# Kernel optimization log

Measured on AMD Instinct MI355X. Metric: run time of the kernel, lower is better.

Reference implementation:

```python
import jax, jax.numpy as jnp
import numpy as np

N = 50_000       # nodes
E = 1_600_000    # edges per edge set (avg degree 32)
D = 128          # hidden dim
F_IN = 1273      # fixed num_features in NetGIN
G = 512          # graphs in batch
STEPS = 6        # Set2Set processing steps
BN_EPS = 1e-5


def setup_inputs() -> dict:
    key = jax.random.key(0)
    ks = iter(jax.random.split(key, 40))
    def rn(shape, fan_in):
        return jax.random.normal(next(ks), shape, jnp.float32) / np.float32(np.sqrt(fan_in))
    inp = {}
    inp["x"] = jax.random.normal(next(ks), (N, F_IN), jnp.float32)
    for i in (1, 2, 3):
        inp[f"edge_index_{i}"] = jax.random.randint(next(ks), (2, E), 0, N, jnp.int32)
    inp["batch"] = jnp.sort(jax.random.randint(next(ks), (N,), 0, G, jnp.int32))
    # GINConv MLPs: layer 1 has input F_IN, layers 2-6 have input D
    inp["conv1_W1"] = rn((3, F_IN, D), F_IN)
    inp["conv1_b1"] = jnp.zeros((3, D), jnp.float32)
    inp["conv_rest_W1"] = rn((5, 3, D, D), D)
    inp["conv_rest_b1"] = jnp.zeros((5, 3, D), jnp.float32)
    inp["conv_W2"] = rn((6, 3, D, D), D)
    inp["conv_b2"] = jnp.zeros((6, 3, D), jnp.float32)
    inp["conv_bn1_g"] = jnp.ones((6, 3, D), jnp.float32)
    inp["conv_bn1_b"] = jnp.zeros((6, 3, D), jnp.float32)
    inp["conv_bn2_g"] = jnp.ones((6, 3, D), jnp.float32)
    inp["conv_bn2_b"] = jnp.zeros((6, 3, D), jnp.float32)
    inp["conv_eps"] = jnp.zeros((6, 3), jnp.float32)  # train_eps=True, init 0
    # fusion MLPs (3*D -> D -> D)
    inp["mlp_W1"] = rn((6, 3 * D, D), 3 * D)
    inp["mlp_b1"] = jnp.zeros((6, D), jnp.float32)
    inp["mlp_bn1_g"] = jnp.ones((6, D), jnp.float32)
    inp["mlp_bn1_b"] = jnp.zeros((6, D), jnp.float32)
    inp["mlp_W2"] = rn((6, D, D), D)
    inp["mlp_b2"] = jnp.zeros((6, D), jnp.float32)
    inp["mlp_bn2_g"] = jnp.ones((6, D), jnp.float32)
    inp["mlp_bn2_b"] = jnp.zeros((6, D), jnp.float32)
    # Set2Set single-layer LSTM: input 2D, hidden D; gate order i,f,g,o
    inp["lstm_Wih"] = rn((4 * D, 2 * D), 2 * D)
    inp["lstm_Whh"] = rn((4 * D, D), D)
    inp["lstm_bih"] = jnp.zeros((4 * D,), jnp.float32)
    inp["lstm_bhh"] = jnp.zeros((4 * D,), jnp.float32)
    inp["fc1_W"] = rn((2 * D, D), 2 * D)
    inp["fc1_b"] = jnp.zeros((D,), jnp.float32)
    inp["fc4_W"] = rn((D, 12), D)
    inp["fc4_b"] = jnp.zeros((12,), jnp.float32)
    return inp


def _bn(x, g, b):
    # BatchNorm1d in training mode: batch statistics (biased var), eps=1e-5
    mu = jnp.mean(x, axis=0)
    var = jnp.var(x, axis=0)
    return g * (x - mu) * jax.lax.rsqrt(var + BN_EPS) + b


def _mlp2(h, W1, b1, g1, bb1, W2, b2, g2, bb2):
    h = jax.nn.relu(_bn(h @ W1 + b1, g1, bb1))
    return jax.nn.relu(_bn(h @ W2 + b2, g2, bb2))


def _gin(h, ei, eps, W1, b1, g1, bb1, W2, b2, g2, bb2):
    # sum-aggregate neighbor features: out[dst] += h[src]
    agg = jax.ops.segment_sum(h[ei[0]], ei[1], num_segments=h.shape[0])
    return _mlp2((1.0 + eps) * h + agg, W1, b1, g1, bb1, W2, b2, g2, bb2)


def _forward(x, conv1_W1, conv1_b1, conv_rest_W1, conv_rest_b1, conv_W2, conv_b2,
             conv_bn1_g, conv_bn1_b, conv_bn2_g, conv_bn2_b, conv_eps,
             mlp_W1, mlp_b1, mlp_bn1_g, mlp_bn1_b, mlp_W2, mlp_b2, mlp_bn2_g, mlp_bn2_b,
             lstm_Wih, lstm_Whh, lstm_bih, lstm_bhh, fc1_W, fc1_b, fc4_W, fc4_b,
             edge_index_1, edge_index_2, edge_index_3, batch):
    edges = (edge_index_1, edge_index_2, edge_index_3)
    h = x
    for l in range(6):
        xs = []
        for k in range(3):
            W1 = conv1_W1[k] if l == 0 else conv_rest_W1[l - 1, k]
            b1 = conv1_b1[k] if l == 0 else conv_rest_b1[l - 1, k]
            xk = jax.nn.relu(_gin(h, edges[k], conv_eps[l, k], W1, b1,
                                  conv_bn1_g[l, k], conv_bn1_b[l, k],
                                  conv_W2[l, k], conv_b2[l, k],
                                  conv_bn2_g[l, k], conv_bn2_b[l, k]))
            xs.append(xk)
        h = _mlp2(jnp.concatenate(xs, axis=-1),
                  mlp_W1[l], mlp_b1[l], mlp_bn1_g[l], mlp_bn1_b[l],
                  mlp_W2[l], mlp_b2[l], mlp_bn2_g[l], mlp_bn2_b[l])
    # Set2Set readout (processing_steps=6)
    q_star = jnp.zeros((G, 2 * D), h.dtype)
    hh = jnp.zeros((G, D), h.dtype)
    cc = jnp.zeros((G, D), h.dtype)
    for _ in range(STEPS):
        gates = q_star @ lstm_Wih.T + hh @ lstm_Whh.T + lstm_bih + lstm_bhh
        i_g, f_g, g_g, o_g = jnp.split(gates, 4, axis=-1)
        cc = jax.nn.sigmoid(f_g) * cc + jax.nn.sigmoid(i_g) * jnp.tanh(g_g)
        hh = jax.nn.sigmoid(o_g) * jnp.tanh(cc)
        q = hh
        e = jnp.sum(h * q[batch], axis=-1)              # [N]
        emax = jax.ops.segment_max(e, batch, num_segments=G)
        ex = jnp.exp(e - emax[batch])
        denom = jax.ops.segment_sum(ex, batch, num_segments=G)
        a = ex / denom[batch]                            # per-graph softmax
        r = jax.ops.segment_sum(a[:, None] * h, batch, num_segments=G)
        q_star = jnp.concatenate([q, r], axis=-1)
    out = jax.nn.relu(q_star @ fc1_W + fc1_b)
    return out @ fc4_W + fc4_b                           # [G, 12]


def reference(x, conv1_W1, conv1_b1, conv_rest_W1, conv_rest_b1, conv_W2, conv_b2,
              conv_bn1_g, conv_bn1_b, conv_bn2_g, conv_bn2_b, conv_eps,
              mlp_W1, mlp_b1, mlp_bn1_g, mlp_bn1_b, mlp_W2, mlp_b2, mlp_bn2_g, mlp_bn2_b,
              lstm_Wih, lstm_Whh, lstm_bih, lstm_bhh, fc1_W, fc1_b, fc4_W, fc4_b,
              edge_index_1, edge_index_2, edge_index_3, batch):
    return _forward(x, conv1_W1, conv1_b1, conv_rest_W1, conv_rest_b1, conv_W2, conv_b2,
                    conv_bn1_g, conv_bn1_b, conv_bn2_g, conv_bn2_b, conv_eps,
                    mlp_W1, mlp_b1, mlp_bn1_g, mlp_bn1_b, mlp_W2, mlp_b2, mlp_bn2_g, mlp_bn2_b,
                    lstm_Wih, lstm_Whh, lstm_bih, lstm_bhh, fc1_W, fc1_b, fc4_W, fc4_b,
                    edge_index_1, edge_index_2, edge_index_3, batch)
```

## Files before the change

kernel.cpp:

```cpp
#include <hip/hip_runtime.h>
#include <cstdint>
#include <cstddef>

#define NN 50000
#define EE 1600000
#define GG 512
#define FIN 1273

typedef unsigned short u16;
typedef unsigned int u32;
typedef __attribute__((ext_vector_type(8))) short short8;
typedef __attribute__((ext_vector_type(4))) float f32x4;

__device__ __forceinline__ float sigmf(float x) { return 1.f / (1.f + expf(-x)); }

__device__ __forceinline__ void splitbf(float v, u16& hi, u16& lo) {
    const u32 u = __float_as_uint(v);
    hi = (u16)(u >> 16);
    const float rem = v - __uint_as_float(u & 0xffff0000u);
    lo = (u16)(__float_as_uint(rem) >> 16);
}

__device__ __forceinline__ void gload_lds16(const void* g, void* l) {
    __builtin_amdgcn_global_load_lds(
        (const __attribute__((address_space(1))) void*)g,
        (__attribute__((address_space(3))) void*)l, 16, 0, 0);
}

__device__ __forceinline__ bool remap3(int f, int nRow, int& mat, int& rt) {
    const int g = f / 24, w = f - g * 24;
    rt = g * 8 + (w & 7);
    mat = w >> 3;
    return rt < nRow;
}

__global__ __launch_bounds__(256) void gemm_l0(
    const float* __restrict__ A, int lda, int K, int Kreal,
    const u16* __restrict__ Bhi, const u16* __restrict__ Blo, size_t strideB,
    float* __restrict__ C, int ldc, int coffStep, int M, int nRow)
{
    __shared__ u16 lsAhi[128 * 64];
    __shared__ u16 lsAlo[128 * 64];
    __shared__ u16 lsBhi[128 * 64];
    __shared__ u16 lsBlo[128 * 64];
    int mat, rt;
    if (!remap3(blockIdx.x, nRow, mat, rt)) return;
    const int tid = threadIdx.x;
    const int wave = tid >> 6, lane = tid & 63;
    const int row0 = rt * 128;
    const int coff = mat * coffStep;
    const u16* Bh = Bhi + (size_t)mat * strideB;
    const u16* Bl = Blo + (size_t)mat * strideB;
    const int wm = wave >> 1, wn = wave & 1;
    f32x4 acc[4][4] = {};

    for (int k0 = 0; k0 < K; k0 += 64) {
        if (k0) __syncthreads();
        #pragma unroll
        for (int i = 0; i < 4; ++i) {
            const int slot = i * 256 + tid;
            const int r = slot >> 3, ch = tid & 7;
            int gr = row0 + r; if (gr >= M) gr = M - 1;
            const int kb = k0 + ch * 8;
            u16 th[8], tl[8];
            const float* src = A + (size_t)gr * lda + kb;
            if (kb + 8 <= Kreal) {
                const float4 v0 = *(const float4*)(src);
                const float4 v1 = *(const float4*)(src + 4);
                const float va[8] = {v0.x, v0.y, v0.z, v0.w,
                                     v1.x, v1.y, v1.z, v1.w};
                #pragma unroll
                for (int e = 0; e < 8; ++e) splitbf(va[e], th[e], tl[e]);
            } else {
                #pragma unroll
                for (int e = 0; e < 8; ++e) {
                    const float v = (kb + e < Kreal) ? src[e] : 0.f;
                    splitbf(v, th[e], tl[e]);
                }
            }
            const int off = (r << 6) + ((ch ^ (r & 7)) << 3);
            *(short8*)&lsAhi[off] = *(const short8*)th;
            *(short8*)&lsAlo[off] = *(const short8*)tl;
        }
        #pragma unroll
        for (int i = 0; i < 4; ++i) {
            const int slot = i * 256 + wave * 64 + lane;
            const int r = slot >> 3, ch = slot & 7;
            const int sch = ch ^ (r & 7);
            const size_t goff = (size_t)r * K + k0 + sch * 8;
            const int lbase = (i * 256 + wave * 64) * 8;
            gload_lds16(Bh + goff, &lsBhi[lbase]);
            gload_lds16(Bl + goff, &lsBlo[lbase]);
        }
        __syncthreads();
        #pragma unroll
        for (int ks = 0; ks < 2; ++ks) {
            short8 ah[4], al[4], bh[4], bl[4];
            const int kch = ks * 4 + (lane >> 4);
            #pragma unroll
            for (int m = 0; m < 4; ++m) {
                const int r = wm * 64 + m * 16 + (lane & 15);
                const int off = (r << 6) + ((kch ^ (r & 7)) << 3);
                ah[m] = *(const short8*)&lsAhi[off];
                al[m] = *(const short8*)&lsAlo[off];
            }
            #pragma unroll
            for (int n = 0; n < 4; ++n) {
                const int c = wn * 64 + n * 16 + (lane & 15);
                const int off = (c << 6) + ((kch ^ (c & 7)) << 3);
                bh[n] = *(const short8*)&lsBhi[off];
                bl[n] = *(const short8*)&lsBlo[off];
            }
            #pragma unroll
            for (int m = 0; m < 4; ++m)
                #pragma unroll
                for (int n = 0; n < 4; ++n) {
                    acc[m][n] = __builtin_amdgcn_mfma_f32_16x16x32_bf16(
                        ah[m], bh[n], acc[m][n], 0, 0, 0);
                    acc[m][n] = __builtin_amdgcn_mfma_f32_16x16x32_bf16(
                        ah[m], bl[n], acc[m][n], 0, 0, 0);
                    acc[m][n] = __builtin_amdgcn_mfma_f32_16x16x32_bf16(
                        al[m], bh[n], acc[m][n], 0, 0, 0);
                }
        }
    }
    #pragma unroll
    for (int n = 0; n < 4; ++n) {
        const int c = wn * 64 + n * 16 + (lane & 15);
        #pragma unroll
        for (int m = 0; m < 4; ++m) {
            #pragma unroll
            for (int j = 0; j < 4; ++j) {
                const int gr = row0 + wm * 64 + m * 16 + ((lane >> 4) << 2) + j;
                if (gr < M)
                    C[(size_t)gr * ldc + coff + c] = acc[m][n][j];
            }
        }
    }
}

__global__ __launch_bounds__(256) void gemm_dir(
    const float* __restrict__ A, size_t strideA, int lda, int K,
    const float* __restrict__ st, int stSlice, int stMat,
    const float* __restrict__ ga, const float* __restrict__ be,
    int gbSlice, int gbMat,
    const u16* __restrict__ Bhi, const u16* __restrict__ Blo, size_t strideB,
    const float* __restrict__ bias, int biasMat,
    float* __restrict__ C, int ldc, int coffStep,
    int M, int do_stats, float* __restrict__ stats_out, int ostatMat,
    int nMat, int nRow)
{
    __shared__ u16 lsBhi[128 * 64];
    __shared__ u16 lsBlo[128 * 64];
    int mat, rt;
    if (nMat == 3) {
        if (!remap3(blockIdx.x, nRow, mat, rt)) return;
    } else { mat = 0; rt = blockIdx.x; }
    const int tid = threadIdx.x;
    const int wave = tid >> 6, lane = tid & 63;
    const int row0 = rt * 128;
    const int wm = wave >> 1, wn = wave & 1;
    A += (size_t)mat * strideA;
    st += mat * stMat; ga += mat * gbMat; be += mat * gbMat;
    if (bias) bias += mat * biasMat;
    if (do_stats) stats_out += mat * ostatMat;
    const u16* Bh = Bhi + (size_t)mat * strideB;
    const u16* Bl = Blo + (size_t)mat * strideB;
    const int coff = mat * coffStep;
    f32x4 acc[4][4] = {};

    int arow[4];
    #pragma unroll
    for (int m = 0; m < 4; ++m) {
        int r = row0 + wm * 64 + m * 16 + (lane & 15);
        if (r >= M) r = M - 1;
        arow[m] = r;
    }

    for (int k0 = 0; k0 < K; k0 += 64) {
        if (k0) __syncthreads();
        #pragma unroll
        for (int i = 0; i < 4; ++i) {
            const int slot = i * 256 + wave * 64 + lane;
            const int r = slot >> 3, ch = slot & 7;
            const int sch = ch ^ (r & 7);
            const size_t goff = (size_t)r * K + k0 + sch * 8;
            const int lbase = (i * 256 + wave * 64) * 8;
            gload_lds16(Bh + goff, &lsBhi[lbase]);
            gload_lds16(Bl + goff, &lsBlo[lbase]);
        }
        __syncthreads();
        #pragma unroll
        for (int ks = 0; ks < 2; ++ks) {
            const int kch = ks * 4 + (lane >> 4);
            const int kb = k0 + kch * 8;
            float scv[8], shv[8];
            {
                const int s = kb >> 7, d0 = kb & 127;
                const float* stS = st + s * stSlice;
                const float* gS  = ga + s * gbSlice;
                const float* beS = be + s * gbSlice;
                #pragma unroll
                for (int e = 0; e < 8; ++e) {
                    const int d = d0 + e;
                    const float mu = stS[d] * (1.f / NN);
                    const float var = fmaxf(stS[128 + d] * (1.f / NN) - mu * mu, 0.f);
                    const float sc = gS[d] * rsqrtf(var + 1e-5f);
                    scv[e] = sc;
                    shv[e] = beS[d] - sc * mu;
                }
            }
            short8 ah[4], al[4];
            #pragma unroll
            for (int m = 0; m < 4; ++m) {
                const float* src = A + (size_t)arow[m] * lda + kb;
                const float4 v0 = *(const float4*)(src);
                const float4 v1 = *(const float4*)(src + 4);
                const float va[8] = {v0.x, v0.y, v0.z, v0.w,
                                     v1.x, v1.y, v1.z, v1.w};
                u16 th[8], tl[8];
                #pragma unroll
                for (int e = 0; e < 8; ++e) {
                    const float y = fmaxf(fmaf(scv[e], va[e], shv[e]), 0.f);
                    splitbf(y, th[e], tl[e]);
                }
                ah[m] = *(const short8*)th;
                al[m] = *(const short8*)tl;
            }
            #pragma unroll
            for (int n = 0; n < 4; ++n) {
                const int c = wn * 64 + n * 16 + (lane & 15);
                const int off = (c << 6) + ((kch ^ (c & 7)) << 3);
                const short8 bh = *(const short8*)&lsBhi[off];
                const short8 bl = *(const short8*)&lsBlo[off];
                #pragma unroll
                for (int m = 0; m < 4; ++m) {
                    acc[m][n] = __builtin_amdgcn_mfma_f32_16x16x32_bf16(
                        ah[m], bh, acc[m][n], 0, 0, 0);
                    acc[m][n] = __builtin_amdgcn_mfma_f32_16x16x32_bf16(
                        ah[m], bl, acc[m][n], 0, 0, 0);
                    acc[m][n] = __builtin_amdgcn_mfma_f32_16x16x32_bf16(
                        al[m], bh, acc[m][n], 0, 0, 0);
                }
            }
        }
    }

    float colsum[4] = {0.f, 0.f, 0.f, 0.f}, colsq[4] = {0.f, 0.f, 0.f, 0.f};
    #pragma unroll
    for (int n = 0; n < 4; ++n) {
        const int c = wn * 64 + n * 16 + (lane & 15);
        const float bv = bias ? bias[c] : 0.f;
        #pragma unroll
        for (int m = 0; m < 4; ++m) {
            #pragma unroll
            for (int j = 0; j < 4; ++j) {
                const int gr = row0 + wm * 64 + m * 16 + ((lane >> 4) << 2) + j;
                if (gr < M) {
                    const float v = acc[m][n][j] + bv;
                    C[(size_t)gr * ldc + coff + c] = v;
                    colsum[n] += v; colsq[n] += v * v;
                }
            }
        }
    }
    if (do_stats) {
        float* ssum = (float*)lsBhi;
        float* ssq  = ssum + 128;
        __syncthreads();
        if (tid < 128) { ssum[tid] = 0.f; ssq[tid] = 0.f; }
        __syncthreads();
        #pragma unroll
        for (int n = 0; n < 4; ++n) {
            const int c = wn * 64 + n * 16 + (lane & 15);
            atomicAdd(&ssum[c], colsum[n]);
            atomicAdd(&ssq[c], colsq[n]);
        }
        __syncthreads();
        if (tid < 128) {
            atomicAdd(&stats_out[tid],       ssum[tid]);
            atomicAdd(&stats_out[128 + tid], ssq[tid]);
        }
    }
}

__global__ __launch_bounds__(256) void wt_cast2(const float* __restrict__ W,
                                                u16* __restrict__ Whi,
                                                u16* __restrict__ Wlo,
                                                int total, int K, int Kpad) {
    const int idx = blockIdx.x * 256 + threadIdx.x;
    if (idx >= total) return;
    const int perm = 128 * Kpad;
    const int m = idx / perm, rem = idx - m * perm;
    const int n = rem / Kpad, k = rem - n * Kpad;
    const float v = (k < K) ? W[(size_t)m * K * 128 + (size_t)k * 128 + n] : 0.f;
    u16 hi, lo;
    splitbf(v, hi, lo);
    Whi[idx] = hi; Wlo[idx] = lo;
}

template <bool BT>
__global__ __launch_bounds__(256) void gemm_f32(
    const float* __restrict__ A, const float* __restrict__ B,
    const float* __restrict__ bias, float* __restrict__ C,
    int M, int K, int Nc)
{
    __shared__ float As[32][68];
    __shared__ float Bs[32][132];
    const int tid = threadIdx.x;
    const int tx = tid & 15, ty = tid >> 4;
    const int row0 = blockIdx.x * 64, col0 = blockIdx.y * 128;
    float acc[4][8] = {};
    for (int k0 = 0; k0 < K; k0 += 32) {
        {
            const int kk = tid & 31, rb = tid >> 5;
            #pragma unroll
            for (int i = 0; i < 8; ++i) {
                const int r = rb + i * 8, gr = row0 + r, gk = k0 + kk;
                As[kk][r] = (gr < M && gk < K) ? A[(size_t)gr * K + gk] : 0.f;
            }
        }
        if (!BT) {
            const int c = tid & 127, kb = tid >> 7;
            #pragma unroll
            for (int i = 0; i < 16; ++i) {
                const int kk = kb + i * 2, gk = k0 + kk;
                Bs[kk][c] = (gk < K) ? B[(size_t)gk * Nc + col0 + c] : 0.f;
            }
        } else {
            const int kk = tid & 31, cb = tid >> 5;
            #pragma unroll
            for (int i = 0; i < 16; ++i) {
                const int c = cb + i * 8, gk = k0 + kk;
                Bs[kk][c] = (gk < K) ? B[(size_t)(col0 + c) * K + gk] : 0.f;
            }
        }
        __syncthreads();
        #pragma unroll 8
        for (int kk = 0; kk < 32; ++kk) {
            const float4 av  = *(const float4*)&As[kk][ty * 4];
            const float4 bv0 = *(const float4*)&Bs[kk][tx * 8];
            const float4 bv1 = *(const float4*)&Bs[kk][tx * 8 + 4];
            const float a[4] = {av.x, av.y, av.z, av.w};
            const float b[8] = {bv0.x, bv0.y, bv0.z, bv0.w, bv1.x, bv1.y, bv1.z, bv1.w};
            #pragma unroll
            for (int i = 0; i < 4; ++i)
                #pragma unroll
                for (int j = 0; j < 8; ++j)
                    acc[i][j] = fmaf(a[i], b[j], acc[i][j]);
        }
        __syncthreads();
    }
    #pragma unroll
    for (int j = 0; j < 8; ++j) {
        const float bv = bias ? bias[col0 + tx * 8 + j] : 0.f;
        #pragma unroll
        for (int i = 0; i < 4; ++i) acc[i][j] += bv;
    }
    #pragma unroll
    for (int i = 0; i < 4; ++i) {
        const int gr = row0 + ty * 4 + i;
        if (gr < M) {
            *(float4*)&C[(size_t)gr * Nc + col0 + tx * 8] =
                make_float4(acc[i][0], acc[i][1], acc[i][2], acc[i][3]);
            *(float4*)&C[(size_t)gr * Nc + col0 + tx * 8 + 4] =
                make_float4(acc[i][4], acc[i][5], acc[i][6], acc[i][7]);
        }
    }
}

__global__ __launch_bounds__(256) void count_deg(const int* __restrict__ dst,
                                                 int* __restrict__ deg) {
    const int e = blockIdx.x * 256 + threadIdx.x;
    if (e < EE) atomicAdd(&deg[dst[e]], 1);
}

__global__ __launch_bounds__(512) void scan1(const int* __restrict__ deg,
                                             int* __restrict__ scanned,
                                             int* __restrict__ bsum) {
    __shared__ int s[512];
    const int t = threadIdx.x;
    const int i = blockIdx.x * 512 + t;
    const int v = (i < NN) ? deg[i] : 0;
    s[t] = v; __syncthreads();
    for (int o = 1; o < 512; o <<= 1) {
        const int tv = (t >= o) ? s[t - o] : 0;
        __syncthreads();
        s[t] += tv;
        __syncthreads();
    }
    if (i < NN) scanned[i] = s[t];
    if (t == 511) bsum[blockIdx.x] = s[511];
}

__global__ __launch_bounds__(128) void scan2(int* __restrict__ bsum, int nb) {
    __shared__ int s[128];
    const int t = threadIdx.x;
    const int v = (t < nb) ? bsum[t] : 0;
    s[t] = v; __syncthreads();
    for (int o = 1; o < 128; o <<= 1) {
        const int tv = (t >= o) ? s[t - o] : 0;
        __syncthreads();
        s[t] += tv;
        __syncthreads();
    }
    if (t < nb) bsum[t] = s[t] - v;
}

__global__ __launch_bounds__(256) void scan3(const int* __restrict__ deg,
                                             const int* __restrict__ scanned,
                                             const int* __restrict__ bsum,
                                             int* __restrict__ rowptr,
                                             int* __restrict__ cursor) {
    const int i = blockIdx.x * 256 + threadIdx.x;
    if (i < NN) {
        const int v = bsum[i >> 9] + scanned[i] - deg[i];
        rowptr[i] = v; cursor[i] = v;
    }
    if (i == 0) rowptr[NN] = EE;
}

__global__ __launch_bounds__(256) void fill_csr(const int* __restrict__ src,
                                                const int* __restrict__ dst,
                                                int* __restrict__ cursor,
                                                int* __restrict__ csrc) {
    const int e = blockIdx.x * 256 + threadIdx.x;
    if (e < EE) {
        const int pos = atomicAdd(&cursor[dst[e]], 1);
        csrc[pos] = src[e];
    }
}

__global__ __launch_bounds__(256) void agg_combine(
    const float* __restrict__ X, int ldp4,
    const int* __restrict__ rowptrB, const int* __restrict__ csrcB,
    const float* __restrict__ b1B,
    const float* __restrict__ eps_arr, int epsBase,
    float* __restrict__ zB, float* __restrict__ statsB)
{
    __shared__ float red[256];
    const int k = blockIdx.y;
    const int* rowptr = rowptrB + (size_t)k * (NN + 1);
    const int* csrc   = csrcB + (size_t)k * EE;
    const float* b1   = b1B + k * 128;
    float* z          = zB + (size_t)k * NN * 128;
    float* stats      = statsB + (size_t)k * 512;
    const int tid = threadIdx.x, lane = tid & 63, wave = tid >> 6;
    const float e1 = 1.f + eps_arr[epsBase + k];
    const int half = lane >> 5;
    const int l32 = lane & 31;
    const float4* p4 = (const float4*)X + k * 32;
    float s[4] = {0.f, 0.f, 0.f, 0.f}, q[4] = {0.f, 0.f, 0.f, 0.f};
    float4 bv = make_float4(0.f, 0.f, 0.f, 0.f);
    if (lane < 32) bv = ((const float4*)b1)[l32];
    red[tid] = 0.f;
    __syncthreads();
    const int nbase = blockIdx.x * 16 + wave * 4;
    for (int t = 0; t < 4; ++t) {
        const int wid = nbase + t;
        const int s0 = rowptr[wid], s1 = rowptr[wid + 1];
        float ax = 0.f, ay = 0.f, az = 0.f, aw = 0.f;
        int j = s0;
        for (; j + 15 < s1; j += 16) {
            const int r0 = csrc[j + half],      r1 = csrc[j + 2 + half];
            const int r2 = csrc[j + 4 + half],  r3 = csrc[j + 6 + half];
            const int r4 = csrc[j + 8 + half],  r5 = csrc[j + 10 + half];
            const int r6 = csrc[j + 12 + half], r7 = csrc[j + 14 + half];
            const float4 v0 = p4[(size_t)r0 * ldp4 + l32];
            const float4 v1 = p4[(size_t)r1 * ldp4 + l32];
            const float4 v2 = p4[(size_t)r2 * ldp4 + l32];
            const float4 v3 = p4[(size_t)r3 * ldp4 + l32];
            const float4 v4 = p4[(size_t)r4 * ldp4 + l32];
            const float4 v5 = p4[(size_t)r5 * ldp4 + l32];
            const float4 v6 = p4[(size_t)r6 * ldp4 + l32];
            const float4 v7 = p4[(size_t)r7 * ldp4 + l32];
            ax += (v0.x + v1.x) + (v2.x + v3.x) + (v4.x + v5.x) + (v6.x + v7.x);
            ay += (v0.y + v1.y) + (v2.y + v3.y) + (v4.y + v5.y) + (v6.y + v7.y);
            az += (v0.z + v1.z) + (v2.z + v3.z) + (v4.z + v5.z) + (v6.z + v7.z);
            aw += (v0.w + v1.w) + (v2.w + v3.w) + (v4.w + v5.w) + (v6.w + v7.w);
        }
        for (; j + 7 < s1; j += 8) {
            const int r0 = csrc[j + half],     r1 = csrc[j + 2 + half];
            const int r2 = csrc[j + 4 + half], r3 = csrc[j + 6 + half];
            const float4 v0 = p4[(size_t)r0 * ldp4 + l32];
            const float4 v1 = p4[(size_t)r1 * ldp4 + l32];
            const float4 v2 = p4[(size_t)r2 * ldp4 + l32];
            const float4 v3 = p4[(size_t)r3 * ldp4 + l32];
            ax += (v0.x + v1.x) + (v2.x + v3.x);
            ay += (v0.y + v1.y) + (v2.y + v3.y);
            az += (v0.z + v1.z) + (v2.z + v3.z);
            aw += (v0.w + v1.w) + (v2.w + v3.w);
        }
        for (; j + 3 < s1; j += 4) {
            const int ra = csrc[j + half];
            const int rb = csrc[j + 2 + half];
            const float4 v0 = p4[(size_t)ra * ldp4 + l32];
            const float4 v1 = p4[(size_t)rb * ldp4 + l32];
            ax += v0.x + v1.x; ay += v0.y + v1.y;
            az += v0.z + v1.z; aw += v0.w + v1.w;
        }
        for (; j + 1 < s1; j += 2) {
            const int ra = csrc[j + half];
            const float4 v0 = p4[(size_t)ra * ldp4 + l32];
            ax += v0.x; ay += v0.y; az += v0.z; aw += v0.w;
        }
        if (j < s1 && half == 0) {
            const float4 v0 = p4[(size_t)csrc[j] * ldp4 + l32];
            ax += v0.x; ay += v0.y; az += v0.z; aw += v0.w;
        }
        ax += __shfl_down(ax, 32, 64);
        ay += __shfl_down(ay, 32, 64);
        az += __shfl_down(az, 32, 64);
        aw += __shfl_down(aw, 32, 64);
        if (lane < 32) {
            const float4 self = p4[(size_t)wid * ldp4 + l32];
            float4 zv;
            zv.x = fmaf(e1, self.x, ax + bv.x);
            zv.y = fmaf(e1, self.y, ay + bv.y);
            zv.z = fmaf(e1, self.z, az + bv.z);
            zv.w = fmaf(e1, self.w, aw + bv.w);
            ((float4*)z)[(size_t)wid * 32 + l32] = zv;
            s[0] += zv.x; s[1] += zv.y; s[2] += zv.z; s[3] += zv.w;
            q[0] += zv.x * zv.x; q[1] += zv.y * zv.y;
            q[2] += zv.z * zv.z; q[3] += zv.w * zv.w;
        }
    }
    if (lane < 32) {
        const int d = l32 * 4;
        #pragma unroll
        for (int c = 0; c < 4; ++c) {
            atomicAdd(&red[d + c], s[c]);
            atomicAdd(&red[128 + d + c], q[c]);
        }
    }
    __syncthreads();
    atomicAdd(&stats[tid], red[tid]);
}

__global__ __launch_bounds__(256) void bn_relu_f32(
    const float* __restrict__ xin, const float* __restrict__ stats,
    const float* __restrict__ gamma, const float* __restrict__ beta,
    float* __restrict__ out)
{
    const size_t i = (size_t)blockIdx.x * 256 + threadIdx.x;
    if (i >= (size_t)NN * 64) return;
    const int d = (int)(i & 63) * 2;
    const float inv_n = 1.f / NN;
    const float mu0 = stats[d] * inv_n,     mu1 = stats[d + 1] * inv_n;
    const float v0 = fmaxf(stats[128 + d] * inv_n - mu0 * mu0, 0.f);
    const float v1 = fmaxf(stats[129 + d] * inv_n - mu1 * mu1, 0.f);
    const float s0 = gamma[d] * rsqrtf(v0 + 1e-5f);
    const float s1 = gamma[d + 1] * rsqrtf(v1 + 1e-5f);
    const float2 xv = ((const float2*)xin)[i];
    const float y0 = fmaxf(fmaf(s0, xv.x - mu0, beta[d]), 0.f);
    const float y1 = fmaxf(fmaf(s1, xv.y - mu1, beta[d + 1]), 0.f);
    ((float2*)out)[i] = make_float2(y0, y1);
}

__global__ __launch_bounds__(256) void seg_starts(const int* __restrict__ batch,
                                                  int* __restrict__ gstart) {
    const int i = blockIdx.x * 256 + threadIdx.x;
    if (i >= NN) return;
    const int b = batch[i];
    if (i == 0) { for (int g = 0; g <= b; ++g) gstart[g] = 0; }
    else {
        const int pb = batch[i - 1];
        for (int g = pb + 1; g <= b; ++g) gstart[g] = i;
    }
    if (i == NN - 1) { for (int g = b + 1; g <= GG; ++g) gstart[g] = NN; }
}

__global__ __launch_bounds__(256) void pack_wcat(const float* __restrict__ Wih,
                                                 const float* __restrict__ Whh,
                                                 float* __restrict__ Wcat) {
    const int i = blockIdx.x * 256 + threadIdx.x;
    if (i >= 512 * 384) return;
    const int j = i / 384, k = i - j * 384;
    Wcat[i] = (k < 256) ? Wih[j * 256 + k] : Whh[j * 128 + (k - 256)];
}

__global__ __launch_bounds__(256) void lstm_kernel(
    const float* __restrict__ gates, const float* __restrict__ bih,
    const float* __restrict__ bhh, float* __restrict__ cc, float* __restrict__ S)
{
    const int i = blockIdx.x * 256 + threadIdx.x;
    if (i >= GG * 128) return;
    const int g = i >> 7, d = i & 127;
    const float* gr = gates + (size_t)g * 512;
    const float ig = gr[d]       + bih[d]       + bhh[d];
    const float fg = gr[128 + d] + bih[128 + d] + bhh[128 + d];
    const float gv = gr[256 + d] + bih[256 + d] + bhh[256 + d];
    const float og = gr[384 + d] + bih[384 + d] + bhh[384 + d];
    const float c  = sigmf(fg) * cc[i] + sigmf(ig) * tanhf(gv);
    const float hv = sigmf(og) * tanhf(c);
    cc[i] = c;
    S[(size_t)g * 384 + d] = hv;
    S[(size_t)g * 384 + 256 + d] = hv;
}

__global__ __launch_bounds__(256) void attend_kernel(
    const float* __restrict__ h, float* __restrict__ S,
    float* __restrict__ ews, const int* __restrict__ gstart)
{
    const int g = blockIdx.x;
    const int rs = gstart[g], re = gstart[g + 1];
    const int tid = threadIdx.x, lane = tid & 63, w = tid >> 6;
    __shared__ float q[128];
    __shared__ float red[8];
    if (tid < 128) q[tid] = S[(size_t)g * 384 + 256 + tid];
    __syncthreads();
    const float2* h2 = (const float2*)h;
    float lmax = -1e30f;
    for (int n = rs + w; n < re; n += 4) {
        const float2 hv = h2[(size_t)n * 64 + lane];
        float p = hv.x * q[2 * lane] + hv.y * q[2 * lane + 1];
        #pragma unroll
        for (int o = 32; o; o >>= 1) p += __shfl_down(p, o, 64);
        if (lane == 0) { ews[n] = p; lmax = fmaxf(lmax, p); }
    }
    if (lane == 0) red[w] = lmax;
    __syncthreads();
    const float m = fmaxf(fmaxf(red[0], red[1]), fmaxf(red[2], red[3]));
    __syncthreads();
    float lsum = 0.f;
    for (int n = rs + tid; n < re; n += 256) {
        const float ex = expf(ews[n] - m);
        ews[n] = ex; lsum += ex;
    }
    #pragma unroll
    for (int o = 32; o; o >>= 1) lsum += __shfl_down(lsum, o, 64);
    if (lane == 0) red[w] = lsum;
    __syncthreads();
    const float denom = red[0] + red[1] + red[2] + red[3];
    if (tid < 128) {
        float acc = 0.f;
        for (int n = rs; n < re; ++n)
            acc = fmaf(ews[n], h[(size_t)n * 128 + tid], acc);
        S[(size_t)g * 384 + 128 + tid] = (denom > 0.f) ? acc / denom : 0.f;
    }
}

__global__ __launch_bounds__(128) void fc1_kernel(const float* __restrict__ S,
                                                  const float* __restrict__ W,
                                                  const float* __restrict__ b,
                                                  float* __restrict__ out1) {
    const int g = blockIdx.x, d = threadIdx.x;
    __shared__ float qs[256];
    qs[d] = S[(size_t)g * 384 + d];
    qs[128 + d] = S[(size_t)g * 384 + 128 + d];
    __syncthreads();
    float acc = b[d];
    for (int k = 0; k < 256; ++k) acc = fmaf(qs[k], W[k * 128 + d], acc);
    out1[(size_t)g * 128 + d] = fmaxf(acc, 0.f);
}

__global__ __launch_bounds__(256) void fc4_kernel(const float* __restrict__ out1,
                                                  const float* __restrict__ W,
                                                  const float* __restrict__ b,
                                                  float* __restrict__ out) {
    const int i = blockIdx.x * 256 + threadIdx.x;
    if (i >= GG * 12) return;
    const int g = i / 12, j = i - g * 12;
    float acc = b[j];
    for (int d = 0; d < 128; ++d)
        acc = fmaf(out1[(size_t)g * 128 + d], W[d * 12 + j], acc);
    out[i] = acc;
}

extern "C" void kernel_launch(void* const* d_in, const int* in_sizes, int n_in,
                              void* d_out, int out_size, void* d_ws, size_t ws_size,
                              hipStream_t stream)
{
    const float* x        = (const float*)d_in[0];
    const int*   eidx[3]  = {(const int*)d_in[1], (const int*)d_in[2], (const int*)d_in[3]};
    const int*   batch    = (const int*)d_in[4];
    const float* conv1_W1     = (const float*)d_in[5];
    const float* conv1_b1     = (const float*)d_in[6];
    const float* conv_rest_W1 = (const float*)d_in[7];
    const float* conv_rest_b1 = (const float*)d_in[8];
    const float* conv_W2      = (const float*)d_in[9];
    const float* conv_b2      = (const float*)d_in[10];
    const float* conv_bn1_g   = (const float*)d_in[11];
    const float* conv_bn1_b   = (const float*)d_in[12];
    const float* conv_bn2_g   = (const float*)d_in[13];
    const float* conv_bn2_b   = (const float*)d_in[14];
    const float* conv_eps     = (const float*)d_in[15];
    const float* mlp_W1       = (const float*)d_in[16];
    const float* mlp_b1       = (const float*)d_in[17];
    const float* mlp_bn1_g    = (const float*)d_in[18];
    const float* mlp_bn1_b    = (const float*)d_in[19];
    const float* mlp_W2       = (const float*)d_in[20];
    const float* mlp_b2       = (const float*)d_in[21];
    const float* mlp_bn2_g    = (const float*)d_in[22];
    const float* mlp_bn2_b    = (const float*)d_in[23];
    const float* lstm_Wih     = (const float*)d_in[24];
    const float* lstm_Whh     = (const float*)d_in[25];
    const float* lstm_bih     = (const float*)d_in[26];
    const float* lstm_bhh     = (const float*)d_in[27];
    const float* fc1_W        = (const float*)d_in[28];
    const float* fc1_b        = (const float*)d_in[29];
    const float* fc4_W        = (const float*)d_in[30];
    const float* fc4_b        = (const float*)d_in[31];
    float* outp = (float*)d_out;

    float* f = (float*)d_ws;
    size_t fo = 0;
    float* X     = f + fo; fo += (size_t)NN * 384;
    float* zs    = f + fo; fo += (size_t)NN * 384;
    float* zm2   = f + fo; fo += (size_t)NN * 128;
    float* ews   = f + fo; fo += NN;
    float* stats = f + fo; fo += 48 * 256;
    float* S     = f + fo; fo += (size_t)GG * 384;
    float* ccb   = f + fo; fo += (size_t)GG * 128;
    float* gates = f + fo; fo += (size_t)GG * 512;
    float* Wcat  = f + fo; fo += (size_t)512 * 384;
    float* hbuf = X;
    fo = (fo + 7) & ~(size_t)7;
    u16* b = (u16*)(f + fo);
    size_t bo = 0;
    u16* c1_hi   = b + bo; bo += (size_t)3 * 128 * 1280;
    u16* c1_lo   = b + bo; bo += (size_t)3 * 128 * 1280;
    u16* rw1_hi  = b + bo; bo += (size_t)15 * 128 * 128;
    u16* rw1_lo  = b + bo; bo += (size_t)15 * 128 * 128;
    u16* w2_hi   = b + bo; bo += (size_t)18 * 128 * 128;
    u16* w2_lo   = b + bo; bo += (size_t)18 * 128 * 128;
    u16* mw1_hi  = b + bo; bo += (size_t)6 * 128 * 384;
    u16* mw1_lo  = b + bo; bo += (size_t)6 * 128 * 384;
    u16* mw2_hi  = b + bo; bo += (size_t)6 * 128 * 128;
    u16* mw2_lo  = b + bo; bo += (size_t)6 * 128 * 128;
    int* ip = (int*)(b + bo);
    size_t io = 0;
    int* rowptr0 = ip + io; io += (size_t)3 * (NN + 1);
    int* csrc0   = ip + io; io += (size_t)3 * EE;
    int* deg     = ip + io; io += NN;
    int* cursor  = ip + io; io += NN;
    int* scanned = ip + io; io += NN;
    int* bsum    = ip + io; io += 128;
    int* gstart  = ip + io; io += GG + 1;
    const size_t need = fo * 4 + bo * 2 + io * 4;
    if (ws_size < need) return;

    const int NBLK_SCAN = (NN + 511) / 512;

    {
        int t;
        t = 3 * 128 * 1280;
        wt_cast2<<<(t + 255) / 256, 256, 0, stream>>>(conv1_W1, c1_hi, c1_lo, t, FIN, 1280);
        t = 15 * 128 * 128;
        wt_cast2<<<(t + 255) / 256, 256, 0, stream>>>(conv_rest_W1, rw1_hi, rw1_lo, t, 128, 128);
        t = 18 * 128 * 128;
        wt_cast2<<<(t + 255) / 256, 256, 0, stream>>>(conv_W2, w2_hi, w2_lo, t, 128, 128);
        t = 6 * 128 * 384;
        wt_cast2<<<(t + 255) / 256, 256, 0, stream>>>(mlp_W1, mw1_hi, mw1_lo, t, 384, 384);
        t = 6 * 128 * 128;
        wt_cast2<<<(t + 255) / 256, 256, 0, stream>>>(mlp_W2, mw2_hi, mw2_lo, t, 128, 128);
    }

    for (int s = 0; s < 3; ++s) {
        int* rowptr = rowptr0 + (size_t)s * (NN + 1);
        int* csrc   = csrc0 + (size_t)s * EE;
        hipMemsetAsync(deg, 0, NN * sizeof(int), stream);
        count_deg<<<(EE + 255) / 256, 256, 0, stream>>>(eidx[s] + EE, deg);
        scan1<<<NBLK_SCAN, 512, 0, stream>>>(deg, scanned, bsum);
        scan2<<<1, 128, 0, stream>>>(bsum, NBLK_SCAN);
        scan3<<<(NN + 255) / 256, 256, 0, stream>>>(deg, scanned, bsum, rowptr, cursor);
        fill_csr<<<(EE + 255) / 256, 256, 0, stream>>>(eidx[s], eidx[s] + EE, cursor, csrc);
    }
    seg_starts<<<(NN + 255) / 256, 256, 0, stream>>>(batch, gstart);
    hipMemsetAsync(stats, 0, 48 * 256 * sizeof(float), stream);
    hipMemsetAsync(S, 0, (size_t)GG * 384 * sizeof(float), stream);
    hipMemsetAsync(ccb, 0, (size_t)GG * 128 * sizeof(float), stream);

    const int G128 = (NN + 127) / 128;
    const int G3   = 24 * ((G128 + 7) / 8);
    const int AGG_GRID = NN / 16;

    for (int l = 0; l < 6; ++l) {
        float* stL    = stats + (size_t)l * 8 * 256;
        float* slotF1 = stL + 6 * 256;
        float* slotF2 = stL + 7 * 256;

        if (l == 0)
            gemm_l0<<<G3, 256, 0, stream>>>(
                x, FIN, 1280, FIN, c1_hi, c1_lo, (size_t)128 * 1280,
                X, 384, 128, NN, G128);
        else
            gemm_dir<<<G3, 256, 0, stream>>>(
                zm2, 0, 128, 128,
                stats + (size_t)((l - 1) * 8 + 7) * 256, 0, 0,
                mlp_bn2_g + (l - 1) * 128, mlp_bn2_b + (l - 1) * 128, 0, 0,
                rw1_hi + (size_t)(l - 1) * 3 * 128 * 128,
                rw1_lo + (size_t)(l - 1) * 3 * 128 * 128, (size_t)128 * 128,
                nullptr, 0, X, 384, 128, NN, 0, nullptr, 0, 3, G128);

        {
            const float* b1B = (l == 0) ? conv1_b1 : conv_rest_b1 + (l - 1) * 3 * 128;
            agg_combine<<<dim3(AGG_GRID, 3), 256, 0, stream>>>(
                X, 96, rowptr0, csrc0, b1B, conv_eps, l * 3, zs, stL);
        }

        gemm_dir<<<G3, 256, 0, stream>>>(
            zs, (size_t)NN * 128, 128, 128,
            stL, 0, 512,
            conv_bn1_g + l * 3 * 128, conv_bn1_b + l * 3 * 128, 0, 128,
            w2_hi + (size_t)l * 3 * 128 * 128,
            w2_lo + (size_t)l * 3 * 128 * 128, (size_t)128 * 128,
            conv_b2 + l * 3 * 128, 128,
            X, 384, 128, NN, 1, stL + 256, 512, 3, G128);

        gemm_dir<<<G128, 256, 0, stream>>>(
            X, 0, 384, 384,
            stL + 256, 512, 0,
            conv_bn2_g + l * 3 * 128, conv_bn2_b + l * 3 * 128, 128, 0,
            mw1_hi + (size_t)l * 128 * 384, mw1_lo + (size_t)l * 128 * 384, 0,
            mlp_b1 + l * 128, 0, zs, 128, 0, NN, 1, slotF1, 0, 1, G128);

        gemm_dir<<<G128, 256, 0, stream>>>(
            zs, 0, 128, 128,
            slotF1, 0, 0,
            mlp_bn1_g + l * 128, mlp_bn1_b + l * 128, 0, 0,
            mw2_hi + (size_t)l * 128 * 128, mw2_lo + (size_t)l * 128 * 128, 0,
            mlp_b2 + l * 128, 0, zm2, 128, 0, NN, 1, slotF2, 0, 1, G128);
    }
    bn_relu_f32<<<(NN * 64 + 255) / 256, 256, 0, stream>>>(
        zm2, stats + (size_t)(5 * 8 + 7) * 256,
        mlp_bn2_g + 5 * 128, mlp_bn2_b + 5 * 128, hbuf);

    pack_wcat<<<(512 * 384 + 255) / 256, 256, 0, stream>>>(lstm_Wih, lstm_Whh, Wcat);
    for (int t = 0; t < 6; ++t) {
        gemm_f32<true><<<dim3(8, 4), 256, 0, stream>>>(
            S, Wcat, nullptr, gates, GG, 384, 512);
        lstm_kernel<<<(GG * 128 + 255) / 256, 256, 0, stream>>>(
            gates, lstm_bih, lstm_bhh, ccb, S);
        attend_kernel<<<GG, 256, 0, stream>>>(hbuf, S, ews, gstart);
    }
    fc1_kernel<<<GG, 128, 0, stream>>>(S, fc1_W, fc1_b, gates);
    fc4_kernel<<<(GG * 12 + 255) / 256, 256, 0, stream>>>(gates, fc4_W, fc4_b, outp);
}
```

Before: 5.202 ms.

## Aggregate before first conv linear for layers 1-5 to shrink gather width

For layers after the first, the neighbor aggregation now gathers 128-wide rows from the previous MLP output, applying its BN+ReLU on the fly, instead of gathering the three 384-wide projected rows. The first conv linear (W1) then runs after aggregation as a per-edge-set GEMM, using linearity, and its stats come from that GEMM's epilogue. This cuts the scattered gather volume per layer and removes the pre-aggregation GEMM, but adds a GEMM step and rearranges buffer use. The first layer keeps the original order.

```diff
diff --git a/kernel.cpp b/kernel.cpp
--- a/kernel.cpp
+++ b/kernel.cpp
@@ -139,6 +139,7 @@
     }
 }
 
+template <int ABN>
 __global__ __launch_bounds__(256) void gemm_dir(
     const float* __restrict__ A, size_t strideA, int lda, int K,
     const float* __restrict__ st, int stSlice, int stMat,
@@ -161,7 +162,7 @@
     const int row0 = rt * 128;
     const int wm = wave >> 1, wn = wave & 1;
     A += (size_t)mat * strideA;
-    st += mat * stMat; ga += mat * gbMat; be += mat * gbMat;
+    if (ABN) { st += mat * stMat; ga += mat * gbMat; be += mat * gbMat; }
     if (bias) bias += mat * biasMat;
     if (do_stats) stats_out += mat * ostatMat;
     const u16* Bh = Bhi + (size_t)mat * strideB;
@@ -195,7 +196,7 @@
             const int kch = ks * 4 + (lane >> 4);
             const int kb = k0 + kch * 8;
             float scv[8], shv[8];
-            {
+            if (ABN) {
                 const int s = kb >> 7, d0 = kb & 127;
                 const float* stS = st + s * stSlice;
                 const float* gS  = ga + s * gbSlice;
@@ -221,7 +222,8 @@
                 u16 th[8], tl[8];
                 #pragma unroll
                 for (int e = 0; e < 8; ++e) {
-                    const float y = fmaxf(fmaf(scv[e], va[e], shv[e]), 0.f);
+                    const float y = ABN
+                        ? fmaxf(fmaf(scv[e], va[e], shv[e]), 0.f) : va[e];
                     splitbf(y, th[e], tl[e]);
                 }
                 ah[m] = *(const short8*)th;
@@ -431,10 +433,13 @@
     }
 }
 
+template <int L0>
 __global__ __launch_bounds__(256) void agg_combine(
     const float* __restrict__ X, int ldp4,
     const int* __restrict__ rowptrB, const int* __restrict__ csrcB,
     const float* __restrict__ b1B,
+    const float* __restrict__ stF2, const float* __restrict__ gam,
+    const float* __restrict__ bet,
     const float* __restrict__ eps_arr, int epsBase,
     float* __restrict__ zB, float* __restrict__ statsB)
 {
@@ -442,19 +447,37 @@
     const int k = blockIdx.y;
     const int* rowptr = rowptrB + (size_t)k * (NN + 1);
     const int* csrc   = csrcB + (size_t)k * EE;
-    const float* b1   = b1B + k * 128;
     float* z          = zB + (size_t)k * NN * 128;
-    float* stats      = statsB + (size_t)k * 512;
     const int tid = threadIdx.x, lane = tid & 63, wave = tid >> 6;
     const float e1 = 1.f + eps_arr[epsBase + k];
     const int half = lane >> 5;
     const int l32 = lane & 31;
-    const float4* p4 = (const float4*)X + k * 32;
+    const float4* p4 = (const float4*)X + (L0 ? k * 32 : 0);
     float s[4] = {0.f, 0.f, 0.f, 0.f}, q[4] = {0.f, 0.f, 0.f, 0.f};
     float4 bv = make_float4(0.f, 0.f, 0.f, 0.f);
-    if (lane < 32) bv = ((const float4*)b1)[l32];
-    red[tid] = 0.f;
-    __syncthreads();
+    float sc[4], sh[4];
+    if (L0) {
+        if (lane < 32) bv = ((const float4*)(b1B + k * 128))[l32];
+    } else {
+        #pragma unroll
+        for (int c = 0; c < 4; ++c) {
+            const int d = l32 * 4 + c;
+            const float mu = stF2[d] * (1.f / NN);
+            const float var = fmaxf(stF2[128 + d] * (1.f / NN) - mu * mu, 0.f);
+            const float s_ = gam[d] * rsqrtf(var + 1e-5f);
+            sc[c] = s_;
+            sh[c] = bet[d] - s_ * mu;
+        }
+    }
+    auto bnv = [&](float4 v) -> float4 {
+        if (L0) return v;
+        v.x = fmaxf(fmaf(sc[0], v.x, sh[0]), 0.f);
+        v.y = fmaxf(fmaf(sc[1], v.y, sh[1]), 0.f);
+        v.z = fmaxf(fmaf(sc[2], v.z, sh[2]), 0.f);
+        v.w = fmaxf(fmaf(sc[3], v.w, sh[3]), 0.f);
+        return v;
+    };
+    if (L0) { red[tid] = 0.f; __syncthreads(); }
     const int nbase = blockIdx.x * 16 + wave * 4;
     for (int t = 0; t < 4; ++t) {
         const int wid = nbase + t;
@@ -466,14 +489,14 @@
             const int r2 = csrc[j + 4 + half],  r3 = csrc[j + 6 + half];
             const int r4 = csrc[j + 8 + half],  r5 = csrc[j + 10 + half];
             const int r6 = csrc[j + 12 + half], r7 = csrc[j + 14 + half];
-            const float4 v0 = p4[(size_t)r0 * ldp4 + l32];
-            const float4 v1 = p4[(size_t)r1 * ldp4 + l32];
-            const float4 v2 = p4[(size_t)r2 * ldp4 + l32];
-            const float4 v3 = p4[(size_t)r3 * ldp4 + l32];
-            const float4 v4 = p4[(size_t)r4 * ldp4 + l32];
-            const float4 v5 = p4[(size_t)r5 * ldp4 + l32];
-            const float4 v6 = p4[(size_t)r6 * ldp4 + l32];
-            const float4 v7 = p4[(size_t)r7 * ldp4 + l32];
+            const float4 v0 = bnv(p4[(size_t)r0 * ldp4 + l32]);
+            const float4 v1 = bnv(p4[(size_t)r1 * ldp4 + l32]);
+            const float4 v2 = bnv(p4[(size_t)r2 * ldp4 + l32]);
+            const float4 v3 = bnv(p4[(size_t)r3 * ldp4 + l32]);
+            const float4 v4 = bnv(p4[(size_t)r4 * ldp4 + l32]);
+            const float4 v5 = bnv(p4[(size_t)r5 * ldp4 + l32]);
+            const float4 v6 = bnv(p4[(size_t)r6 * ldp4 + l32]);
+            const float4 v7 = bnv(p4[(size_t)r7 * ldp4 + l32]);
             ax += (v0.x + v1.x) + (v2.x + v3.x) + (v4.x + v5.x) + (v6.x + v7.x);
             ay += (v0.y + v1.y) + (v2.y + v3.y) + (v4.y + v5.y) + (v6.y + v7.y);
             az += (v0.z + v1.z) + (v2.z + v3.z) + (v4.z + v5.z) + (v6.z + v7.z);
@@ -482,30 +505,27 @@
         for (; j + 7 < s1; j += 8) {
             const int r0 = csrc[j + half],     r1 = csrc[j + 2 + half];
             const int r2 = csrc[j + 4 + half], r3 = csrc[j + 6 + half];
-            const float4 v0 = p4[(size_t)r0 * ldp4 + l32];
-            const float4 v1 = p4[(size_t)r1 * ldp4 + l32];
-            const float4 v2 = p4[(size_t)r2 * ldp4 + l32];
-            const float4 v3 = p4[(size_t)r3 * ldp4 + l32];
+            const float4 v0 = bnv(p4[(size_t)r0 * ldp4 + l32]);
+            const float4 v1 = bnv(p4[(size_t)r1 * ldp4 + l32]);
+            const float4 v2 = bnv(p4[(size_t)r2 * ldp4 + l32]);
+            const float4 v3 = bnv(p4[(size_t)r3 * ldp4 + l32]);
             ax += (v0.x + v1.x) + (v2.x + v3.x);
             ay += (v0.y + v1.y) + (v2.y + v3.y);
             az += (v0.z + v1.z) + (v2.z + v3.z);
             aw += (v0.w + v1.w) + (v2.w + v3.w);
         }
         for (; j + 3 < s1; j += 4) {
-            const int ra = csrc[j + half];
-            const int rb = csrc[j + 2 + half];
-            const float4 v0 = p4[(size_t)ra * ldp4 + l32];
-            const float4 v1 = p4[(size_t)rb * ldp4 + l32];
+            const float4 v0 = bnv(p4[(size_t)csrc[j + half] * ldp4 + l32]);
+            const float4 v1 = bnv(p4[(size_t)csrc[j + 2 + half] * ldp4 + l32]);
             ax += v0.x + v1.x; ay += v0.y + v1.y;
             az += v0.z + v1.z; aw += v0.w + v1.w;
         }
         for (; j + 1 < s1; j += 2) {
-            const int ra = csrc[j + half];
-            const float4 v0 = p4[(size_t)ra * ldp4 + l32];
+            const float4 v0 = bnv(p4[(size_t)csrc[j + half] * ldp4 + l32]);
             ax += v0.x; ay += v0.y; az += v0.z; aw += v0.w;
         }
         if (j < s1 && half == 0) {
-            const float4 v0 = p4[(size_t)csrc[j] * ldp4 + l32];
+            const float4 v0 = bnv(p4[(size_t)csrc[j] * ldp4 + l32]);
             ax += v0.x; ay += v0.y; az += v0.z; aw += v0.w;
         }
         ax += __shfl_down(ax, 32, 64);
@@ -513,28 +533,32 @@
         az += __shfl_down(az, 32, 64);
         aw += __shfl_down(aw, 32, 64);
         if (lane < 32) {
-            const float4 self = p4[(size_t)wid * ldp4 + l32];
+            const float4 self = bnv(p4[(size_t)wid * ldp4 + l32]);
             float4 zv;
             zv.x = fmaf(e1, self.x, ax + bv.x);
             zv.y = fmaf(e1, self.y, ay + bv.y);
             zv.z = fmaf(e1, self.z, az + bv.z);
             zv.w = fmaf(e1, self.w, aw + bv.w);
             ((float4*)z)[(size_t)wid * 32 + l32] = zv;
-            s[0] += zv.x; s[1] += zv.y; s[2] += zv.z; s[3] += zv.w;
-            q[0] += zv.x * zv.x; q[1] += zv.y * zv.y;
-            q[2] += zv.z * zv.z; q[3] += zv.w * zv.w;
-        }
-    }
-    if (lane < 32) {
-        const int d = l32 * 4;
-        #pragma unroll
-        for (int c = 0; c < 4; ++c) {
-            atomicAdd(&red[d + c], s[c]);
-            atomicAdd(&red[128 + d + c], q[c]);
-        }
-    }
-    __syncthreads();
-    atomicAdd(&stats[tid], red[tid]);
+            if (L0) {
+                s[0] += zv.x; s[1] += zv.y; s[2] += zv.z; s[3] += zv.w;
+                q[0] += zv.x * zv.x; q[1] += zv.y * zv.y;
+                q[2] += zv.z * zv.z; q[3] += zv.w * zv.w;
+            }
+        }
+    }
+    if (L0) {
+        if (lane < 32) {
+            const int d = l32 * 4;
+            #pragma unroll
+            for (int c = 0; c < 4; ++c) {
+                atomicAdd(&red[d + c], s[c]);
+                atomicAdd(&red[128 + d + c], q[c]);
+            }
+        }
+        __syncthreads();
+        atomicAdd(&statsB[(size_t)k * 512 + tid], red[tid]);
+    }
 }
 
 __global__ __launch_bounds__(256) void bn_relu_f32(
@@ -706,7 +730,7 @@
     float* f = (float*)d_ws;
     size_t fo = 0;
     float* X     = f + fo; fo += (size_t)NN * 384;
-    float* zs    = f + fo; fo += (size_t)NN * 384;
+    float* sb    = f + fo; fo += (size_t)NN * 384;
     float* zm2   = f + fo; fo += (size_t)NN * 128;
     float* ews   = f + fo; fo += NN;
     float* stats = f + fo; fo += 48 * 256;
@@ -714,7 +738,6 @@
     float* ccb   = f + fo; fo += (size_t)GG * 128;
     float* gates = f + fo; fo += (size_t)GG * 512;
     float* Wcat  = f + fo; fo += (size_t)512 * 384;
-    float* hbuf = X;
     fo = (fo + 7) & ~(size_t)7;
     u16* b = (u16*)(f + fo);
     size_t bo = 0;
@@ -779,44 +802,56 @@
         float* stL    = stats + (size_t)l * 8 * 256;
         float* slotF1 = stL + 6 * 256;
         float* slotF2 = stL + 7 * 256;
-
-        if (l == 0)
+        float* mlp1in  = (l == 0) ? X : sb;
+        float* mlp1out = (l == 0) ? sb : X;
+
+        if (l == 0) {
             gemm_l0<<<G3, 256, 0, stream>>>(
                 x, FIN, 1280, FIN, c1_hi, c1_lo, (size_t)128 * 1280,
                 X, 384, 128, NN, G128);
-        else
-            gemm_dir<<<G3, 256, 0, stream>>>(
-                zm2, 0, 128, 128,
-                stats + (size_t)((l - 1) * 8 + 7) * 256, 0, 0,
-                mlp_bn2_g + (l - 1) * 128, mlp_bn2_b + (l - 1) * 128, 0, 0,
+            agg_combine<1><<<dim3(AGG_GRID, 3), 256, 0, stream>>>(
+                X, 96, rowptr0, csrc0, conv1_b1,
+                nullptr, nullptr, nullptr, conv_eps, 0, sb, stL);
+            gemm_dir<1><<<G3, 256, 0, stream>>>(
+                sb, (size_t)NN * 128, 128, 128,
+                stL, 0, 512,
+                conv_bn1_g + l * 3 * 128, conv_bn1_b + l * 3 * 128, 0, 128,
+                w2_hi + (size_t)l * 3 * 128 * 128,
+                w2_lo + (size_t)l * 3 * 128 * 128, (size_t)128 * 128,
+                conv_b2 + l * 3 * 128, 128,
+                X, 384, 128, NN, 1, stL + 256, 512, 3, G128);
+        } else {
+            agg_combine<0><<<dim3(AGG_GRID, 3), 256, 0, stream>>>(
+                zm2, 32, rowptr0, csrc0, nullptr,
+                stats + (size_t)((l - 1) * 8 + 7) * 256,
+                mlp_bn2_g + (l - 1) * 128, mlp_bn2_b + (l - 1) * 128,
+                conv_eps, l * 3, sb, nullptr);
+            gemm_dir<0><<<G3, 256, 0, stream>>>(
+                sb, (size_t)NN * 128, 128, 128,
+                nullptr, 0, 0, nullptr, nullptr, 0, 0,
                 rw1_hi + (size_t)(l - 1) * 3 * 128 * 128,
                 rw1_lo + (size_t)(l - 1) * 3 * 128 * 128, (size_t)128 * 128,
-                nullptr, 0, X, 384, 128, NN, 0, nullptr, 0, 3, G128);
-
-        {
-            const float* b1B = (l == 0) ? conv1_b1 : conv_rest_b1 + (l - 1) * 3 * 128;
-            agg_combine<<<dim3(AGG_GRID, 3), 256, 0, stream>>>(
-                X, 96, rowptr0, csrc0, b1B, conv_eps, l * 3, zs, stL);
-        }
-
-        gemm_dir<<<G3, 256, 0, stream>>>(
-            zs, (size_t)NN * 128, 128, 128,
-            stL, 0, 512,
-            conv_bn1_g + l * 3 * 128, conv_bn1_b + l * 3 * 128, 0, 128,
-            w2_hi + (size_t)l * 3 * 128 * 128,
-            w2_lo + (size_t)l * 3 * 128 * 128, (size_t)128 * 128,
-            conv_b2 + l * 3 * 128, 128,
-            X, 384, 128, NN, 1, stL + 256, 512, 3, G128);
-
-        gemm_dir<<<G128, 256, 0, stream>>>(
-            X, 0, 384, 384,
+                conv_rest_b1 + (l - 1) * 3 * 128, 128,
+                X, 384, 128, NN, 1, stL, 512, 3, G128);
+            gemm_dir<1><<<G3, 256, 0, stream>>>(
+                X, 128, 384, 128,
+                stL, 0, 512,
+                conv_bn1_g + l * 3 * 128, conv_bn1_b + l * 3 * 128, 0, 128,
+                w2_hi + (size_t)l * 3 * 128 * 128,
+                w2_lo + (size_t)l * 3 * 128 * 128, (size_t)128 * 128,
+                conv_b2 + l * 3 * 128, 128,
+                sb, 384, 128, NN, 1, stL + 256, 512, 3, G128);
+        }
+
+        gemm_dir<1><<<G128, 256, 0, stream>>>(
+            mlp1in, 0, 384, 384,
             stL + 256, 512, 0,
             conv_bn2_g + l * 3 * 128, conv_bn2_b + l * 3 * 128, 128, 0,
             mw1_hi + (size_t)l * 128 * 384, mw1_lo + (size_t)l * 128 * 384, 0,
-            mlp_b1 + l * 128, 0, zs, 128, 0, NN, 1, slotF1, 0, 1, G128);
-
-        gemm_dir<<<G128, 256, 0, stream>>>(
-            zs, 0, 128, 128,
+            mlp_b1 + l * 128, 0, mlp1out, 128, 0, NN, 1, slotF1, 0, 1, G128);
+
+        gemm_dir<1><<<G128, 256, 0, stream>>>(
+            mlp1out, 0, 128, 128,
             slotF1, 0, 0,
             mlp_bn1_g + l * 128, mlp_bn1_b + l * 128, 0, 0,
             mw2_hi + (size_t)l * 128 * 128, mw2_lo + (size_t)l * 128 * 128, 0,
@@ -824,7 +859,7 @@
     }
     bn_relu_f32<<<(NN * 64 + 255) / 256, 256, 0, stream>>>(
         zm2, stats + (size_t)(5 * 8 + 7) * 256,
-        mlp_bn2_g + 5 * 128, mlp_bn2_b + 5 * 128, hbuf);
+        mlp_bn2_g + 5 * 128, mlp_bn2_b + 5 * 128, X);
 
     pack_wcat<<<(512 * 384 + 255) / 256, 256, 0, stream>>>(lstm_Wih, lstm_Whh, Wcat);
     for (int t = 0; t < 6; ++t) {
@@ -832,7 +867,7 @@
             S, Wcat, nullptr, gates, GG, 384, 512);
         lstm_kernel<<<(GG * 128 + 255) / 256, 256, 0, stream>>>(
             gates, lstm_bih, lstm_bhh, ccb, S);
-        attend_kernel<<<GG, 256, 0, stream>>>(hbuf, S, ews, gstart);
+        attend_kernel<<<GG, 256, 0, stream>>>(X, S, ews, gstart);
     }
     fc1_kernel<<<GG, 128, 0, stream>>>(S, fc1_W, fc1_b, gates);
     fc4_kernel<<<(GG * 12 + 255) / 256, 256, 0, stream>>>(gates, fc4_W, fc4_b, outp);
```

Result: faster. 5.021 ms (-3.5%).
